# Kernel optimization log

Hardware: AMD Instinct MI355X
Metric: run time of the kernel (lower is better)

The kernel has to match this reference:

```python
import jax, jax.numpy as jnp
import numpy as np
import math

D_MODEL = 768
B, S = 8, 2048


def setup_inputs() -> dict:
    key = jax.random.key(0)
    k1, k2, k3, k4, k5 = jax.random.split(key, 5)
    return {
        "input": jax.random.normal(k1, (B, S, D_MODEL), dtype=jnp.float32),
        "attention_mask": jax.random.randint(k2, (B,), 0, S + 1, dtype=jnp.int32),
        "Wq": jax.random.normal(k3, (D_MODEL, D_MODEL), dtype=jnp.float32),
        "Wk": jax.random.normal(k4, (D_MODEL, D_MODEL), dtype=jnp.float32),
        "Wv": jax.random.normal(k5, (D_MODEL, D_MODEL), dtype=jnp.float32),
    }


def reference(input, attention_mask, Wq, Wk, Wv):
    d_model = Wq.shape[0]
    # QKV projections (v is computed in the original but never used in the output)
    q = jnp.matmul(input, Wq)  # [B,S,D]
    k = jnp.matmul(input, Wk)  # [B,S,D]
    v = jnp.matmul(input, Wv)  # [B,S,D] (dead in original forward output)
    # Per-sample QK^T, vectorized instead of the original python loop+cat
    attention_score = jnp.einsum("bqd,bkd->bqk", q, k) / math.sqrt(float(d_model) ** 3)
    # Ragged mask: positions (j,k) with j<len_i and k<len_i keep the score, else -1000.
    # Built with vectorized arange comparisons instead of the original triple python loop.
    idx = jnp.arange(attention_score.shape[1])  # [S]
    valid = idx[None, :] < attention_mask[:, None]  # [B,S]
    keep = valid[:, :, None] & valid[:, None, :]  # [B,S,S]
    mask_attention_score = jnp.where(keep, attention_score, jnp.float32(-1000.0))
    attention_score_n = jax.nn.softmax(mask_attention_score, axis=-1)  # computed but unused, as in original
    # Original returns UNMASKED, pre-softmax scores matmul'd with the raw input (not v).
    self_attention = jnp.einsum("bqk,bkd->bqd", attention_score, input)
    return self_attention
```

## Files before the change

kernel.cpp:

```cpp
#include <hip/hip_runtime.h>
#include <cmath>


typedef __attribute__((ext_vector_type(8))) short short8;
typedef __attribute__((ext_vector_type(4))) float f32x4;

__device__ __forceinline__ unsigned short f2bf(float f) {
    union { float f; unsigned int u; } v; v.f = f;
    unsigned int u = v.u;
    return (unsigned short)((u + 0x7FFFu + ((u >> 16) & 1u)) >> 16);
}

template <int ROWS>
__device__ __forceinline__ void stage_glds(const unsigned short* src, unsigned short* lds,
                                           int ld, int tid)
{
    #pragma unroll
    for (int it = 0; it < ROWS / 32; ++it) {
        int slot = it * 256 + tid;
        int r = slot >> 3, c = slot & 7;
        const unsigned short* gp = src + (size_t)r * ld + ((c ^ (r & 7)) << 3);
        unsigned short* lp = lds + (size_t)(it * 256 + (tid & 192)) * 8;
        __builtin_amdgcn_global_load_lds(
            (__attribute__((address_space(1))) void*)(void*)gp,
            (__attribute__((address_space(3))) void*)lp, 16, 0, 0);
    }
}

template <int ROWS>
__device__ __forceinline__ void stage_f32(const float* __restrict__ src, unsigned short* lds,
                                          int ld, int tid)
{
    #pragma unroll
    for (int it = 0; it < ROWS / 32; ++it) {
        int slot = it * 256 + tid;
        int r = slot >> 3, c = slot & 7;
        const float* gp = src + (size_t)r * ld + c * 8;
        float4 a = *reinterpret_cast<const float4*>(gp);
        float4 d = *reinterpret_cast<const float4*>(gp + 4);
        union { short8 s; unsigned short u[8]; } v;
        v.u[0] = f2bf(a.x); v.u[1] = f2bf(a.y); v.u[2] = f2bf(a.z); v.u[3] = f2bf(a.w);
        v.u[4] = f2bf(d.x); v.u[5] = f2bf(d.y); v.u[6] = f2bf(d.z); v.u[7] = f2bf(d.w);
        *reinterpret_cast<short8*>(&lds[r * 64 + ((c ^ (r & 7)) << 3)]) = v.s;
    }
}

template <int ROWS>
__device__ __forceinline__ void stage_f32pair(const float* __restrict__ a,
                                              const float* __restrict__ b,
                                              unsigned short* lds, int ld, int tid)
{
    #pragma unroll
    for (int it = 0; it < ROWS / 32; ++it) {
        int slot = it * 256 + tid;
        int r = slot >> 3, c = slot & 7;
        size_t off = (size_t)r * ld + c * 8;
        float4 a0 = *reinterpret_cast<const float4*>(a + off);
        float4 a1 = *reinterpret_cast<const float4*>(a + off + 4);
        float4 b0 = *reinterpret_cast<const float4*>(b + off);
        float4 b1 = *reinterpret_cast<const float4*>(b + off + 4);
        union { short8 s; unsigned short u[8]; } v;
        v.u[0] = f2bf(a0.x + b0.x); v.u[1] = f2bf(a0.y + b0.y);
        v.u[2] = f2bf(a0.z + b0.z); v.u[3] = f2bf(a0.w + b0.w);
        v.u[4] = f2bf(a1.x + b1.x); v.u[5] = f2bf(a1.y + b1.y);
        v.u[6] = f2bf(a1.z + b1.z); v.u[7] = f2bf(a1.w + b1.w);
        *reinterpret_cast<short8*>(&lds[r * 64 + ((c ^ (r & 7)) << 3)]) = v.s;
    }
}

template <int TM, int TN>
__device__ __forceinline__ void mfma_step(const unsigned short* __restrict__ Al,
                                          const unsigned short* __restrict__ Bl,
                                          f32x4 (&acc)[TM / 32][TN / 32],
                                          int wr, int wc, int l15, int quad)
{
    constexpr int FM = TM / 32, FN = TN / 32;
    short8 af[FM][2], bfr[FN][2];
    #pragma unroll
    for (int i = 0; i < FM; ++i) {
        int ra = wr + i * 16 + l15;
        af[i][0] = *reinterpret_cast<const short8*>(&Al[ra * 64 + ((quad ^ (ra & 7)) << 3)]);
        af[i][1] = *reinterpret_cast<const short8*>(&Al[ra * 64 + (((quad + 4) ^ (ra & 7)) << 3)]);
    }
    #pragma unroll
    for (int i = 0; i < FN; ++i) {
        int rb = wc + i * 16 + l15;
        bfr[i][0] = *reinterpret_cast<const short8*>(&Bl[rb * 64 + ((quad ^ (rb & 7)) << 3)]);
        bfr[i][1] = *reinterpret_cast<const short8*>(&Bl[rb * 64 + (((quad + 4) ^ (rb & 7)) << 3)]);
    }
    #pragma unroll
    for (int ks = 0; ks < 2; ++ks)
        #pragma unroll
        for (int mi = 0; mi < FM; ++mi)
            #pragma unroll
            for (int ni = 0; ni < FN; ++ni)
                acc[mi][ni] = __builtin_amdgcn_mfma_f32_16x16x32_bf16(
                    af[mi][ks], bfr[ni][ks], acc[mi][ni], 0, 0, 0);
}

__device__ __forceinline__ void store_c(float* C, size_t i, float v) { C[i] = v; }
__device__ __forceinline__ void store_c(unsigned short* C, size_t i, float v) { C[i] = f2bf(v); }

template <int TM, int TN, typename CT>
__device__ __forceinline__ void epilogue(CT* __restrict__ C, f32x4 (&acc)[TM / 32][TN / 32],
                                         int rowBase, int colBase, int ldc, float alpha,
                                         int wr, int wc, int l15, int quad)
{
    #pragma unroll
    for (int mi = 0; mi < TM / 32; ++mi)
        #pragma unroll
        for (int ni = 0; ni < TN / 32; ++ni) {
            int col = colBase + wc + ni * 16 + l15;
            #pragma unroll
            for (int r = 0; r < 4; ++r) {
                int row = rowBase + wr + mi * 16 + quad * 4 + r;
                store_c(C, (size_t)row * ldc + col, alpha * acc[mi][ni][r]);
            }
        }
}

__global__ __launch_bounds__(256)
void prep(const float* __restrict__ X, unsigned short* __restrict__ Xt,
          unsigned short* __restrict__ Xbf)
{
    __shared__ unsigned short T[64 * 64];
    const int blk = blockIdx.x;
    const int b = blk & 7;
    const int tile = blk >> 3;
    const int s0 = (tile & 31) * 64;
    const int d0 = (tile >> 5) * 64;
    const float* Xb = X + (size_t)b * 2048 * 768;
    unsigned short* Xtb = Xt + (size_t)b * 2048 * 768;
    unsigned short* Xbb = Xbf + (size_t)b * 2048 * 768;

    const int mr = threadIdx.x >> 4;
    const int mc = threadIdx.x & 15;

    const float* src = &Xb[(size_t)(s0 + 4 * mr) * 768 + d0 + 4 * mc];
    float4 v0 = *reinterpret_cast<const float4*>(src);
    float4 v1 = *reinterpret_cast<const float4*>(src + 768);
    float4 v2 = *reinterpret_cast<const float4*>(src + 2 * 768);
    float4 v3 = *reinterpret_cast<const float4*>(src + 3 * 768);
    ushort4 r0 = { f2bf(v0.x), f2bf(v0.y), f2bf(v0.z), f2bf(v0.w) };
    ushort4 r1 = { f2bf(v1.x), f2bf(v1.y), f2bf(v1.z), f2bf(v1.w) };
    ushort4 r2 = { f2bf(v2.x), f2bf(v2.y), f2bf(v2.z), f2bf(v2.w) };
    ushort4 r3 = { f2bf(v3.x), f2bf(v3.y), f2bf(v3.z), f2bf(v3.w) };
    unsigned short* dstb = &Xbb[(size_t)(s0 + 4 * mr) * 768 + d0 + 4 * mc];
    *reinterpret_cast<ushort4*>(dstb)            = r0;
    *reinterpret_cast<ushort4*>(dstb + 768)      = r1;
    *reinterpret_cast<ushort4*>(dstb + 2 * 768)  = r2;
    *reinterpret_cast<ushort4*>(dstb + 3 * 768)  = r3;

    ushort4 c0 = { r0.x, r1.x, r2.x, r3.x };
    ushort4 c1 = { r0.y, r1.y, r2.y, r3.y };
    ushort4 c2 = { r0.z, r1.z, r2.z, r3.z };
    ushort4 c3 = { r0.w, r1.w, r2.w, r3.w };
    {
        int d;
        d = 4 * mc + 0; *reinterpret_cast<ushort4*>(&T[d * 64 + ((mr ^ (2 * (d & 7))) & 15) * 4]) = c0;
        d = 4 * mc + 1; *reinterpret_cast<ushort4*>(&T[d * 64 + ((mr ^ (2 * (d & 7))) & 15) * 4]) = c1;
        d = 4 * mc + 2; *reinterpret_cast<ushort4*>(&T[d * 64 + ((mr ^ (2 * (d & 7))) & 15) * 4]) = c2;
        d = 4 * mc + 3; *reinterpret_cast<ushort4*>(&T[d * 64 + ((mr ^ (2 * (d & 7))) & 15) * 4]) = c3;
    }
    __syncthreads();
    #pragma unroll
    for (int p = 0; p < 2; ++p) {
        int d  = p * 32 + (threadIdx.x >> 3);
        int q0 = 2 * (threadIdx.x & 7);
        int c  = (q0 ^ (2 * (d & 7))) & 15;
        short8 o = *reinterpret_cast<const short8*>(&T[d * 64 + c * 4]);
        *reinterpret_cast<short8*>(&Xtb[(size_t)(d0 + d) * 2048 + s0 + q0 * 4]) = o;
    }
}

__global__ __launch_bounds__(256)
void gemm_GP(const unsigned short* __restrict__ Xt, float* __restrict__ Ga,
             float* __restrict__ Gb, const float* __restrict__ Wq,
             const float* __restrict__ Wk, unsigned short* __restrict__ P16)
{
    __shared__ unsigned short lds[(96 + 96) * 64];
    const int blk = blockIdx.x;
    const int tid = threadIdx.x, lane = tid & 63, wave = tid >> 6;
    const int l15 = lane & 15, quad = lane >> 4;

    if (blk < 576) {
        const int b  = blk & 7;
        const int ks = (blk >> 3) & 1;
        const int u  = blk >> 4;
        int ty = 0, rem = u, len = 8;
        while (rem >= len) { rem -= len; --len; ++ty; }
        const int tz = ty + rem;
        const int wr = (wave >> 1) * 48, wc = (wave & 1) * 48;

        const unsigned short* Xtb = Xt + (size_t)b * 768 * 2048;
        const unsigned short* A0 = Xtb + (size_t)ty * 96 * 2048 + ks * 1024;
        const unsigned short* B0 = Xtb + (size_t)tz * 96 * 2048 + ks * 1024;
        float* C = (ks ? Gb : Ga) + (size_t)b * 768 * 768;

        f32x4 acc[3][3] = {};
        for (int k0 = 0; k0 < 1024; k0 += 64) {
            stage_glds<96>(A0 + k0, lds, 2048, tid);
            stage_glds<96>(B0 + k0, lds + 96 * 64, 2048, tid);
            __syncthreads();
            mfma_step<96, 96>(lds, lds + 96 * 64, acc, wr, wc, l15, quad);
            __syncthreads();
        }
        #pragma unroll
        for (int mi = 0; mi < 3; ++mi)
            #pragma unroll
            for (int ni = 0; ni < 3; ++ni) {
                int col = tz * 96 + wc + ni * 16 + l15;
                int row0 = ty * 96 + wr + mi * 16 + quad * 4;
                #pragma unroll
                for (int r = 0; r < 4; ++r)
                    C[(size_t)(row0 + r) * 768 + col] = acc[mi][ni][r];
                if (ty < tz) {
                    float4 m = { acc[mi][ni][0], acc[mi][ni][1],
                                 acc[mi][ni][2], acc[mi][ni][3] };
                    *reinterpret_cast<float4*>(&C[(size_t)col * 768 + row0]) = m;
                }
            }
    } else {
        const int pb = blk - 576;
        const int ty = pb / 12, tz = pb - ty * 12;
        const int wr = (wave >> 1) * 32, wc = (wave & 1) * 32;
        f32x4 acc[2][2] = {};
        for (int k0 = 0; k0 < 768; k0 += 64) {
            stage_f32<64>(Wq + (size_t)ty * 64 * 768 + k0, lds, 768, tid);
            stage_f32<64>(Wk + (size_t)tz * 64 * 768 + k0, lds + 64 * 64, 768, tid);
            __syncthreads();
            mfma_step<64, 64>(lds, lds + 64 * 64, acc, wr, wc, l15, quad);
            __syncthreads();
        }
        epilogue<64, 64, unsigned short>(P16, acc, ty * 64, tz * 64, 768, 1.0f,
                                         wr, wc, l15, quad);
    }
}

__global__ __launch_bounds__(256)
void gemm_Ht(const float* __restrict__ Ga, const float* __restrict__ Gb,
             const unsigned short* __restrict__ P16, unsigned short* __restrict__ Ht,
             float alpha)
{
    __shared__ unsigned short lds[(96 + 96) * 64];
    const int b = blockIdx.x, ty = blockIdx.y, tz = blockIdx.z;
    const int tid = threadIdx.x, lane = tid & 63, wave = tid >> 6;
    const int wr = (wave >> 1) * 48, wc = (wave & 1) * 48;
    const int l15 = lane & 15, quad = lane >> 4;

    const float* Ab = Ga + (size_t)b * 768 * 768 + (size_t)ty * 96 * 768;
    const float* Bb = Gb + (size_t)b * 768 * 768 + (size_t)ty * 96 * 768;
    const unsigned short* B0 = P16 + (size_t)tz * 96 * 768;

    f32x4 acc[3][3] = {};
    for (int k0 = 0; k0 < 768; k0 += 64) {
        stage_f32pair<96>(Ab + k0, Bb + k0, lds, 768, tid);
        stage_glds<96>(B0 + k0, lds + 96 * 64, 768, tid);
        __syncthreads();
        mfma_step<96, 96>(lds, lds + 96 * 64, acc, wr, wc, l15, quad);
        __syncthreads();
    }
    epilogue<96, 96, unsigned short>(Ht + (size_t)b * 768 * 768, acc,
                                     ty * 96, tz * 96, 768, alpha, wr, wc, l15, quad);
}

__global__ __launch_bounds__(256)
void gemm_out(const unsigned short* __restrict__ Xbf, const unsigned short* __restrict__ Ht,
              float* __restrict__ out)
{
    __shared__ unsigned short lds[(128 + 128) * 64];
    const int b = blockIdx.x, ty = blockIdx.y, tz = blockIdx.z;
    const int tid = threadIdx.x, lane = tid & 63, wave = tid >> 6;
    const int wr = (wave >> 1) * 64, wc = (wave & 1) * 64;
    const int l15 = lane & 15, quad = lane >> 4;

    const unsigned short* A0 = Xbf + (size_t)b * 2048 * 768 + (size_t)ty * 128 * 768;
    const unsigned short* B0 = Ht + (size_t)b * 768 * 768 + (size_t)tz * 128 * 768;

    f32x4 acc[4][4] = {};
    for (int k0 = 0; k0 < 768; k0 += 64) {
        stage_glds<128>(A0 + k0, lds, 768, tid);
        stage_glds<128>(B0 + k0, lds + 128 * 64, 768, tid);
        __syncthreads();
        mfma_step<128, 128>(lds, lds + 128 * 64, acc, wr, wc, l15, quad);
        __syncthreads();
    }
    epilogue<128, 128, float>(out + (size_t)b * 2048 * 768, acc,
                              ty * 128, tz * 128, 768, 1.0f, wr, wc, l15, quad);
}

extern "C" void kernel_launch(void* const* d_in, const int* in_sizes, int n_in,
                              void* d_out, int out_size, void* d_ws, size_t ws_size,
                              hipStream_t stream)
{
    const float* X  = (const float*)d_in[0];
    const float* Wq = (const float*)d_in[2];
    const float* Wk = (const float*)d_in[3];
    float* out = (float*)d_out;

    const int Bn = 8, S = 2048, D = 768;
    const float alpha = 1.0f / (768.0f * sqrtf(768.0f));
    const size_t szX  = (size_t)Bn * S * D;
    const size_t szDD = (size_t)Bn * D * D;

    unsigned short* Xt  = (unsigned short*)d_ws;
    unsigned short* Xbf = Xt + szX;
    unsigned short* P16 = Xbf + szX;
    float* Ga = (float*)(P16 + (size_t)D * D);
    float* Gb = Ga + szDD;
    unsigned short* Ht = (unsigned short*)(Gb + szDD);

    prep<<<dim3(Bn * (S / 64) * (D / 64)), 256, 0, stream>>>(X, Xt, Xbf);

    gemm_GP<<<dim3(576 + 144), 256, 0, stream>>>(Xt, Ga, Gb, Wq, Wk, P16);

    gemm_Ht<<<dim3(Bn, 8, 8), 256, 0, stream>>>(Ga, Gb, P16, Ht, alpha);

    gemm_out<<<dim3(Bn, S / 128, 6), 256, 0, stream>>>(Xbf, Ht, out);
}
```

Before: 194.2 us.

## Double-buffer LDS in all GEMMs, move Wq·Wkᵀ into prep, share diagonal Gram tiles

All three GEMM kernels now keep two LDS buffers, so the global-to-LDS load for the next k-tile is issued before the MFMAs on the current tile. This removes one barrier per iteration and hides load latency. Global pointers and LDS fragment offsets are now computed once, outside the k-loop. The Wq·Wkᵀ product (P16) moves from the Gram kernel into the prep kernel, and diagonal Gram tiles load the shared operand only once. Doubling LDS per block may lower occupancy, especially for gemm_out, which now uses 64KB.

```diff
diff --git a/kernel.cpp b/kernel.cpp
--- a/kernel.cpp
+++ b/kernel.cpp
@@ -11,20 +11,66 @@
     return (unsigned short)((u + 0x7FFFu + ((u >> 16) & 1u)) >> 16);
 }
 
-template <int ROWS>
-__device__ __forceinline__ void stage_glds(const unsigned short* src, unsigned short* lds,
-                                           int ld, int tid)
-{
-    #pragma unroll
-    for (int it = 0; it < ROWS / 32; ++it) {
-        int slot = it * 256 + tid;
-        int r = slot >> 3, c = slot & 7;
-        const unsigned short* gp = src + (size_t)r * ld + ((c ^ (r & 7)) << 3);
-        unsigned short* lp = lds + (size_t)(it * 256 + (tid & 192)) * 8;
+template <int NIT>
+__device__ __forceinline__ void setup_stage(const unsigned short* base, int ld, int tid,
+                                            const unsigned short* (&gp)[NIT])
+{
+    #pragma unroll
+    for (int it = 0; it < NIT; ++it) {
+        int slot = it * 256 + tid, r = slot >> 3, c = slot & 7;
+        gp[it] = base + (size_t)r * ld + ((c ^ (r & 7)) << 3);
+    }
+}
+
+template <int NIT>
+__device__ __forceinline__ void stage_adv(const unsigned short* const (&gp)[NIT], int koff,
+                                          unsigned short* ldsbase, int tid)
+{
+    #pragma unroll
+    for (int it = 0; it < NIT; ++it) {
+        unsigned short* lp = ldsbase + (size_t)(it * 256 + (tid & 192)) * 8;
         __builtin_amdgcn_global_load_lds(
-            (__attribute__((address_space(1))) void*)(void*)gp,
+            (__attribute__((address_space(1))) void*)(void*)(gp[it] + koff),
             (__attribute__((address_space(3))) void*)lp, 16, 0, 0);
     }
+}
+
+template <int F>
+__device__ __forceinline__ void frag_offs(int wbase, int l15, int quad, int (&o)[F][2])
+{
+    #pragma unroll
+    for (int i = 0; i < F; ++i) {
+        int r = wbase + i * 16 + l15;
+        o[i][0] = r * 64 + ((quad ^ (r & 7)) << 3);
+        o[i][1] = r * 64 + (((quad + 4) ^ (r & 7)) << 3);
+    }
+}
+
+template <int FM, int FN>
+__device__ __forceinline__ void mfma_frags(const unsigned short* __restrict__ Al,
+                                           const unsigned short* __restrict__ Bl,
+                                           const int (&oA)[FM][2], const int (&oB)[FN][2],
+                                           f32x4 (&acc)[FM][FN])
+{
+    short8 af[FM][2], bfr[FN][2];
+    #pragma unroll
+    for (int i = 0; i < FM; ++i) {
+        af[i][0] = *reinterpret_cast<const short8*>(&Al[oA[i][0]]);
+        af[i][1] = *reinterpret_cast<const short8*>(&Al[oA[i][1]]);
+    }
+    #pragma unroll
+    for (int i = 0; i < FN; ++i) {
+        bfr[i][0] = *reinterpret_cast<const short8*>(&Bl[oB[i][0]]);
+        bfr[i][1] = *reinterpret_cast<const short8*>(&Bl[oB[i][1]]);
+    }
+    #pragma unroll
+    for (int ks = 0; ks < 2; ++ks)
+        #pragma unroll
+        for (int mi = 0; mi < FM; ++mi)
+            #pragma unroll
+            for (int ni = 0; ni < FN; ++ni)
+                acc[mi][ni] = __builtin_amdgcn_mfma_f32_16x16x32_bf16(
+                    af[mi][ks], bfr[ni][ks], acc[mi][ni], 0, 0, 0);
 }
 
 template <int ROWS>
@@ -45,59 +91,6 @@
     }
 }
 
-template <int ROWS>
-__device__ __forceinline__ void stage_f32pair(const float* __restrict__ a,
-                                              const float* __restrict__ b,
-                                              unsigned short* lds, int ld, int tid)
-{
-    #pragma unroll
-    for (int it = 0; it < ROWS / 32; ++it) {
-        int slot = it * 256 + tid;
-        int r = slot >> 3, c = slot & 7;
-        size_t off = (size_t)r * ld + c * 8;
-        float4 a0 = *reinterpret_cast<const float4*>(a + off);
-        float4 a1 = *reinterpret_cast<const float4*>(a + off + 4);
-        float4 b0 = *reinterpret_cast<const float4*>(b + off);
-        float4 b1 = *reinterpret_cast<const float4*>(b + off + 4);
-        union { short8 s; unsigned short u[8]; } v;
-        v.u[0] = f2bf(a0.x + b0.x); v.u[1] = f2bf(a0.y + b0.y);
-        v.u[2] = f2bf(a0.z + b0.z); v.u[3] = f2bf(a0.w + b0.w);
-        v.u[4] = f2bf(a1.x + b1.x); v.u[5] = f2bf(a1.y + b1.y);
-        v.u[6] = f2bf(a1.z + b1.z); v.u[7] = f2bf(a1.w + b1.w);
-        *reinterpret_cast<short8*>(&lds[r * 64 + ((c ^ (r & 7)) << 3)]) = v.s;
-    }
-}
-
-template <int TM, int TN>
-__device__ __forceinline__ void mfma_step(const unsigned short* __restrict__ Al,
-                                          const unsigned short* __restrict__ Bl,
-                                          f32x4 (&acc)[TM / 32][TN / 32],
-                                          int wr, int wc, int l15, int quad)
-{
-    constexpr int FM = TM / 32, FN = TN / 32;
-    short8 af[FM][2], bfr[FN][2];
-    #pragma unroll
-    for (int i = 0; i < FM; ++i) {
-        int ra = wr + i * 16 + l15;
-        af[i][0] = *reinterpret_cast<const short8*>(&Al[ra * 64 + ((quad ^ (ra & 7)) << 3)]);
-        af[i][1] = *reinterpret_cast<const short8*>(&Al[ra * 64 + (((quad + 4) ^ (ra & 7)) << 3)]);
-    }
-    #pragma unroll
-    for (int i = 0; i < FN; ++i) {
-        int rb = wc + i * 16 + l15;
-        bfr[i][0] = *reinterpret_cast<const short8*>(&Bl[rb * 64 + ((quad ^ (rb & 7)) << 3)]);
-        bfr[i][1] = *reinterpret_cast<const short8*>(&Bl[rb * 64 + (((quad + 4) ^ (rb & 7)) << 3)]);
-    }
-    #pragma unroll
-    for (int ks = 0; ks < 2; ++ks)
-        #pragma unroll
-        for (int mi = 0; mi < FM; ++mi)
-            #pragma unroll
-            for (int ni = 0; ni < FN; ++ni)
-                acc[mi][ni] = __builtin_amdgcn_mfma_f32_16x16x32_bf16(
-                    af[mi][ks], bfr[ni][ks], acc[mi][ni], 0, 0, 0);
-}
-
 __device__ __forceinline__ void store_c(float* C, size_t i, float v) { C[i] = v; }
 __device__ __forceinline__ void store_c(unsigned short* C, size_t i, float v) { C[i] = f2bf(v); }
 
@@ -120,18 +113,43 @@
 }
 
 __global__ __launch_bounds__(256)
-void prep(const float* __restrict__ X, unsigned short* __restrict__ Xt,
-          unsigned short* __restrict__ Xbf)
-{
-    __shared__ unsigned short T[64 * 64];
+void prep(const float* __restrict__ X, const float* __restrict__ Wq,
+          const float* __restrict__ Wk, unsigned short* __restrict__ Xt,
+          unsigned short* __restrict__ Xbf, unsigned short* __restrict__ P16)
+{
+    __shared__ unsigned short lds[(64 + 64) * 64];
     const int blk = blockIdx.x;
-    const int b = blk & 7;
-    const int tile = blk >> 3;
+    const int tid = threadIdx.x, lane = tid & 63, wave = tid >> 6;
+    const int l15 = lane & 15, quad = lane >> 4;
+
+    if (blk < 144) {
+        const int ty = blk / 12, tz = blk - ty * 12;
+        const int wr = (wave >> 1) * 32, wc = (wave & 1) * 32;
+        int oA[2][2], oB[2][2];
+        frag_offs<2>(wr, l15, quad, oA);
+        frag_offs<2>(wc, l15, quad, oB);
+        f32x4 acc[2][2] = {};
+        for (int k0 = 0; k0 < 768; k0 += 64) {
+            stage_f32<64>(Wq + (size_t)ty * 64 * 768 + k0, lds, 768, tid);
+            stage_f32<64>(Wk + (size_t)tz * 64 * 768 + k0, lds + 64 * 64, 768, tid);
+            __syncthreads();
+            mfma_frags<2, 2>(lds, lds + 64 * 64, oA, oB, acc);
+            __syncthreads();
+        }
+        epilogue<64, 64, unsigned short>(P16, acc, ty * 64, tz * 64, 768, 1.0f,
+                                         wr, wc, l15, quad);
+        return;
+    }
+
+    const int t0 = blk - 144;
+    const int b = t0 & 7;
+    const int tile = t0 >> 3;
     const int s0 = (tile & 31) * 64;
     const int d0 = (tile >> 5) * 64;
     const float* Xb = X + (size_t)b * 2048 * 768;
     unsigned short* Xtb = Xt + (size_t)b * 2048 * 768;
     unsigned short* Xbb = Xbf + (size_t)b * 2048 * 768;
+    unsigned short* T = lds;
 
     const int mr = threadIdx.x >> 4;
     const int mc = threadIdx.x & 15;
@@ -174,67 +192,67 @@
 }
 
 __global__ __launch_bounds__(256)
-void gemm_GP(const unsigned short* __restrict__ Xt, float* __restrict__ Ga,
-             float* __restrict__ Gb, const float* __restrict__ Wq,
-             const float* __restrict__ Wk, unsigned short* __restrict__ P16)
-{
-    __shared__ unsigned short lds[(96 + 96) * 64];
+void gemm_G(const unsigned short* __restrict__ Xt, float* __restrict__ Ga,
+            float* __restrict__ Gb)
+{
+    __shared__ unsigned short lds[2][(96 + 96) * 64];
     const int blk = blockIdx.x;
+    const int b  = blk & 7;
+    const int ks = (blk >> 3) & 1;
+    const int u  = blk >> 4;
+    int ty = 0, rem = u, len = 8;
+    while (rem >= len) { rem -= len; --len; ++ty; }
+    const int tz = ty + rem;
+    const bool diag = (ty == tz);
+
     const int tid = threadIdx.x, lane = tid & 63, wave = tid >> 6;
+    const int wr = (wave >> 1) * 48, wc = (wave & 1) * 48;
     const int l15 = lane & 15, quad = lane >> 4;
 
-    if (blk < 576) {
-        const int b  = blk & 7;
-        const int ks = (blk >> 3) & 1;
-        const int u  = blk >> 4;
-        int ty = 0, rem = u, len = 8;
-        while (rem >= len) { rem -= len; --len; ++ty; }
-        const int tz = ty + rem;
-        const int wr = (wave >> 1) * 48, wc = (wave & 1) * 48;
-
-        const unsigned short* Xtb = Xt + (size_t)b * 768 * 2048;
-        const unsigned short* A0 = Xtb + (size_t)ty * 96 * 2048 + ks * 1024;
-        const unsigned short* B0 = Xtb + (size_t)tz * 96 * 2048 + ks * 1024;
-        float* C = (ks ? Gb : Ga) + (size_t)b * 768 * 768;
-
-        f32x4 acc[3][3] = {};
-        for (int k0 = 0; k0 < 1024; k0 += 64) {
-            stage_glds<96>(A0 + k0, lds, 2048, tid);
-            stage_glds<96>(B0 + k0, lds + 96 * 64, 2048, tid);
-            __syncthreads();
-            mfma_step<96, 96>(lds, lds + 96 * 64, acc, wr, wc, l15, quad);
-            __syncthreads();
-        }
+    const unsigned short* Xtb = Xt + (size_t)b * 768 * 2048;
+    const unsigned short* A0 = Xtb + (size_t)ty * 96 * 2048 + ks * 1024;
+    const unsigned short* B0 = Xtb + (size_t)tz * 96 * 2048 + ks * 1024;
+    float* C = (ks ? Gb : Ga) + (size_t)b * 768 * 768;
+
+    const unsigned short* gA[3]; const unsigned short* gB[3];
+    setup_stage<3>(A0, 2048, tid, gA);
+    setup_stage<3>(B0, 2048, tid, gB);
+    int oA[3][2], oB[3][2];
+    frag_offs<3>(wr, l15, quad, oA);
+    frag_offs<3>(wc, l15, quad, oB);
+    const int bbase = diag ? 0 : 96 * 64;
+
+    f32x4 acc[3][3] = {};
+    stage_adv<3>(gA, 0, &lds[0][0], tid);
+    if (!diag) stage_adv<3>(gB, 0, &lds[0][96 * 64], tid);
+    __syncthreads();
+
+    const int nt = 16;
+    for (int t = 0; t < nt; ++t) {
+        const int cur = t & 1;
+        if (t + 1 < nt) {
+            stage_adv<3>(gA, (t + 1) * 64, &lds[cur ^ 1][0], tid);
+            if (!diag) stage_adv<3>(gB, (t + 1) * 64, &lds[cur ^ 1][96 * 64], tid);
+        }
+        mfma_frags<3, 3>(&lds[cur][0], &lds[cur][bbase], oA, oB, acc);
+        __syncthreads();
+    }
+
+    #pragma unroll
+    for (int mi = 0; mi < 3; ++mi)
         #pragma unroll
-        for (int mi = 0; mi < 3; ++mi)
+        for (int ni = 0; ni < 3; ++ni) {
+            int col = tz * 96 + wc + ni * 16 + l15;
+            int row0 = ty * 96 + wr + mi * 16 + quad * 4;
             #pragma unroll
-            for (int ni = 0; ni < 3; ++ni) {
-                int col = tz * 96 + wc + ni * 16 + l15;
-                int row0 = ty * 96 + wr + mi * 16 + quad * 4;
-                #pragma unroll
-                for (int r = 0; r < 4; ++r)
-                    C[(size_t)(row0 + r) * 768 + col] = acc[mi][ni][r];
-                if (ty < tz) {
-                    float4 m = { acc[mi][ni][0], acc[mi][ni][1],
-                                 acc[mi][ni][2], acc[mi][ni][3] };
-                    *reinterpret_cast<float4*>(&C[(size_t)col * 768 + row0]) = m;
-                }
+            for (int r = 0; r < 4; ++r)
+                C[(size_t)(row0 + r) * 768 + col] = acc[mi][ni][r];
+            if (!diag) {
+                float4 m = { acc[mi][ni][0], acc[mi][ni][1],
+                             acc[mi][ni][2], acc[mi][ni][3] };
+                *reinterpret_cast<float4*>(&C[(size_t)col * 768 + row0]) = m;
             }
-    } else {
-        const int pb = blk - 576;
-        const int ty = pb / 12, tz = pb - ty * 12;
-        const int wr = (wave >> 1) * 32, wc = (wave & 1) * 32;
-        f32x4 acc[2][2] = {};
-        for (int k0 = 0; k0 < 768; k0 += 64) {
-            stage_f32<64>(Wq + (size_t)ty * 64 * 768 + k0, lds, 768, tid);
-            stage_f32<64>(Wk + (size_t)tz * 64 * 768 + k0, lds + 64 * 64, 768, tid);
-            __syncthreads();
-            mfma_step<64, 64>(lds, lds + 64 * 64, acc, wr, wc, l15, quad);
-            __syncthreads();
-        }
-        epilogue<64, 64, unsigned short>(P16, acc, ty * 64, tz * 64, 768, 1.0f,
-                                         wr, wc, l15, quad);
-    }
+        }
 }
 
 __global__ __launch_bounds__(256)
@@ -242,7 +260,7 @@
              const unsigned short* __restrict__ P16, unsigned short* __restrict__ Ht,
              float alpha)
 {
-    __shared__ unsigned short lds[(96 + 96) * 64];
+    __shared__ unsigned short lds[2][(96 + 96) * 64];
     const int b = blockIdx.x, ty = blockIdx.y, tz = blockIdx.z;
     const int tid = threadIdx.x, lane = tid & 63, wave = tid >> 6;
     const int wr = (wave >> 1) * 48, wc = (wave & 1) * 48;
@@ -252,12 +270,49 @@
     const float* Bb = Gb + (size_t)b * 768 * 768 + (size_t)ty * 96 * 768;
     const unsigned short* B0 = P16 + (size_t)tz * 96 * 768;
 
+    size_t pOff[3]; int pLds[3];
+    #pragma unroll
+    for (int it = 0; it < 3; ++it) {
+        int slot = it * 256 + tid, r = slot >> 3, c = slot & 7;
+        pOff[it] = (size_t)r * 768 + c * 8;
+        pLds[it] = r * 64 + ((c ^ (r & 7)) << 3);
+    }
+    const unsigned short* gB[3];
+    setup_stage<3>(B0, 768, tid, gB);
+    int oA[3][2], oB[3][2];
+    frag_offs<3>(wr, l15, quad, oA);
+    frag_offs<3>(wc, l15, quad, oB);
+
+    auto pair_stage = [&](int koff, unsigned short* dst) {
+        #pragma unroll
+        for (int it = 0; it < 3; ++it) {
+            size_t off = pOff[it] + koff;
+            float4 a0 = *reinterpret_cast<const float4*>(Ab + off);
+            float4 a1 = *reinterpret_cast<const float4*>(Ab + off + 4);
+            float4 b0 = *reinterpret_cast<const float4*>(Bb + off);
+            float4 b1 = *reinterpret_cast<const float4*>(Bb + off + 4);
+            union { short8 s; unsigned short u[8]; } v;
+            v.u[0] = f2bf(a0.x + b0.x); v.u[1] = f2bf(a0.y + b0.y);
+            v.u[2] = f2bf(a0.z + b0.z); v.u[3] = f2bf(a0.w + b0.w);
+            v.u[4] = f2bf(a1.x + b1.x); v.u[5] = f2bf(a1.y + b1.y);
+            v.u[6] = f2bf(a1.z + b1.z); v.u[7] = f2bf(a1.w + b1.w);
+            *reinterpret_cast<short8*>(&dst[pLds[it]]) = v.s;
+        }
+    };
+
     f32x4 acc[3][3] = {};
-    for (int k0 = 0; k0 < 768; k0 += 64) {
-        stage_f32pair<96>(Ab + k0, Bb + k0, lds, 768, tid);
-        stage_glds<96>(B0 + k0, lds + 96 * 64, 768, tid);
-        __syncthreads();
-        mfma_step<96, 96>(lds, lds + 96 * 64, acc, wr, wc, l15, quad);
+    pair_stage(0, &lds[0][0]);
+    stage_adv<3>(gB, 0, &lds[0][96 * 64], tid);
+    __syncthreads();
+
+    const int nt = 12;
+    for (int t = 0; t < nt; ++t) {
+        const int cur = t & 1;
+        if (t + 1 < nt) {
+            stage_adv<3>(gB, (t + 1) * 64, &lds[cur ^ 1][96 * 64], tid);
+            pair_stage((t + 1) * 64, &lds[cur ^ 1][0]);
+        }
+        mfma_frags<3, 3>(&lds[cur][0], &lds[cur][96 * 64], oA, oB, acc);
         __syncthreads();
     }
     epilogue<96, 96, unsigned short>(Ht + (size_t)b * 768 * 768, acc,
@@ -268,7 +323,7 @@
 void gemm_out(const unsigned short* __restrict__ Xbf, const unsigned short* __restrict__ Ht,
               float* __restrict__ out)
 {
-    __shared__ unsigned short lds[(128 + 128) * 64];
+    __shared__ unsigned short lds[2][(128 + 128) * 64];
     const int b = blockIdx.x, ty = blockIdx.y, tz = blockIdx.z;
     const int tid = threadIdx.x, lane = tid & 63, wave = tid >> 6;
     const int wr = (wave >> 1) * 64, wc = (wave & 1) * 64;
@@ -277,12 +332,26 @@
     const unsigned short* A0 = Xbf + (size_t)b * 2048 * 768 + (size_t)ty * 128 * 768;
     const unsigned short* B0 = Ht + (size_t)b * 768 * 768 + (size_t)tz * 128 * 768;
 
+    const unsigned short* gA[4]; const unsigned short* gB[4];
+    setup_stage<4>(A0, 768, tid, gA);
+    setup_stage<4>(B0, 768, tid, gB);
+    int oA[4][2], oB[4][2];
+    frag_offs<4>(wr, l15, quad, oA);
+    frag_offs<4>(wc, l15, quad, oB);
+
     f32x4 acc[4][4] = {};
-    for (int k0 = 0; k0 < 768; k0 += 64) {
-        stage_glds<128>(A0 + k0, lds, 768, tid);
-        stage_glds<128>(B0 + k0, lds + 128 * 64, 768, tid);
-        __syncthreads();
-        mfma_step<128, 128>(lds, lds + 128 * 64, acc, wr, wc, l15, quad);
+    stage_adv<4>(gA, 0, &lds[0][0], tid);
+    stage_adv<4>(gB, 0, &lds[0][128 * 64], tid);
+    __syncthreads();
+
+    const int nt = 12;
+    for (int t = 0; t < nt; ++t) {
+        const int cur = t & 1;
+        if (t + 1 < nt) {
+            stage_adv<4>(gA, (t + 1) * 64, &lds[cur ^ 1][0], tid);
+            stage_adv<4>(gB, (t + 1) * 64, &lds[cur ^ 1][128 * 64], tid);
+        }
+        mfma_frags<4, 4>(&lds[cur][0], &lds[cur][128 * 64], oA, oB, acc);
         __syncthreads();
     }
     epilogue<128, 128, float>(out + (size_t)b * 2048 * 768, acc,
@@ -310,9 +379,9 @@
     float* Gb = Ga + szDD;
     unsigned short* Ht = (unsigned short*)(Gb + szDD);
 
-    prep<<<dim3(Bn * (S / 64) * (D / 64)), 256, 0, stream>>>(X, Xt, Xbf);
-
-    gemm_GP<<<dim3(576 + 144), 256, 0, stream>>>(Xt, Ga, Gb, Wq, Wk, P16);
+    prep<<<dim3(144 + Bn * (S / 64) * (D / 64)), 256, 0, stream>>>(X, Wq, Wk, Xt, Xbf, P16);
+
+    gemm_G<<<dim3(576), 256, 0, stream>>>(Xt, Ga, Gb);
 
     gemm_Ht<<<dim3(Bn, 8, 8), 256, 0, stream>>>(Ga, Gb, P16, Ht, alpha);
 
```

Result: faster. 184.0 us (-5.3%).
